# Kernel optimization log

Hardware: AMD Instinct MI355X
Metric: run time of the kernel (lower is better)

Reference implementation:

```python
import jax, jax.numpy as jnp
import numpy as np

CLIP_LENGTH = 256.0
NUM_CLASSES = 21
OVERLAP_THRESH = 0.5
GAMMA = 2.0
ALPHA = 0.25
EPS = float(np.finfo(np.float32).eps)

B, K, N_GT = 32, 32768, 32


def setup_inputs() -> dict:
    key = jax.random.key(0)
    ks = jax.random.split(key, 9)
    loc_data = jax.random.uniform(ks[0], (B, K, 2), jnp.float32) * 64.0 + 1.0  # frame-unit offsets
    conf_data = jax.random.normal(ks[1], (B, K, NUM_CLASSES), jnp.float32)
    prop_loc_data = jax.random.normal(ks[2], (B, K, 2), jnp.float32)
    prop_conf_data = jax.random.normal(ks[3], (B, K, NUM_CLASSES), jnp.float32)
    center_data = jax.random.normal(ks[4], (B, K, 1), jnp.float32)
    priors = jax.random.uniform(ks[5], (K, 1), jnp.float32)  # normalized centers in [0,1]
    t0 = jax.random.uniform(ks[6], (B, N_GT), jnp.float32) * 0.8
    dur = jax.random.uniform(ks[7], (B, N_GT), jnp.float32) * 0.18 + 0.02
    t1 = jnp.minimum(t0 + dur, 1.0)
    labels = jax.random.randint(ks[8], (B, N_GT), 1, NUM_CLASSES).astype(jnp.float32)
    targets = jnp.stack([t0, t1, labels], axis=-1)  # [B, N, 3]
    return {"loc_data": loc_data, "conf_data": conf_data, "prop_loc_data": prop_loc_data,
            "prop_conf_data": prop_conf_data, "center_data": center_data,
            "priors": priors, "targets": targets}


def _calc_iou(pred, target):
    pl, pr = pred[..., 0], pred[..., 1]
    tl, tr = target[..., 0], target[..., 1]
    inter = jnp.minimum(pl, tl) + jnp.minimum(pr, tr)
    union = (pl + pr) + (tl + tr) - inter
    return inter / jnp.maximum(union, EPS)


def _giou_loss(pred, target):
    pl, pr = pred[..., 0], pred[..., 1]
    tl, tr = target[..., 0], target[..., 1]
    inter = jnp.minimum(pl, tl) + jnp.minimum(pr, tr)
    union = (pl + pr) + (tl + tr) - inter
    ious = inter / jnp.maximum(union, EPS)
    ac = jnp.maximum(pl, tl) + jnp.maximum(pr, tr)
    gious = ious - (ac - union) / jnp.maximum(ac, EPS)
    return 1.0 - gious


_ALPHA_VEC = jnp.full((NUM_CLASSES,), 1.0 - ALPHA, jnp.float32).at[0].set(ALPHA)


def _focal_sum(logits, tgt):
    # FocalLoss_Ori with pre-softmax inside MultiSegmentLoss; reduction=sum
    probs = jax.nn.softmax(logits, axis=-1)
    pt = jnp.take_along_axis(probs, tgt[..., None], axis=-1)[..., 0] + 1e-10
    return (-_ALPHA_VEC[tgt] * (1.0 - pt) ** GAMMA * jnp.log(pt)).sum()


def _match_targets(loc_data_ng, priors, targets):
    # everything here mirrors the torch.no_grad() matching block
    truths = targets[..., :2]                       # [B,N,2]
    labels = targets[..., 2].astype(jnp.int32)      # [B,N]
    center = priors[:, 0]                           # [K]
    left = (center[None, :, None] - truths[:, None, :, 0]) * CLIP_LENGTH   # [B,K,N]
    right = (truths[:, None, :, 1] - center[None, :, None]) * CLIP_LENGTH  # [B,K,N]
    maxn = CLIP_LENGTH * 2.0
    area = jnp.where((left < 0) | (right < 0), maxn, left + right)
    best_area = area.min(-1)                        # [B,K]
    best_idx = area.argmin(-1)                      # [B,K]
    t0 = jnp.take_along_axis(truths[..., 0], best_idx, axis=1)
    t1 = jnp.take_along_axis(truths[..., 1], best_idx, axis=1)
    loc_t = jnp.stack([(center[None, :] - t0) * CLIP_LENGTH,
                       (t1 - center[None, :]) * CLIP_LENGTH], axis=-1)     # [B,K,2]
    conf_t = jnp.take_along_axis(labels, best_idx, axis=1)
    conf_t = jnp.where(best_area >= maxn, 0, conf_t)                       # [B,K]
    iou = _calc_iou(loc_data_ng, loc_t)
    prop_conf_t = jnp.where(iou < OVERLAP_THRESH, 0, conf_t)
    prop_w = loc_data_ng[..., 0] + loc_data_ng[..., 1]
    prop_loc_t = (loc_t - loc_data_ng) / (0.5 * prop_w[..., None])
    return loc_t, conf_t, prop_loc_t, prop_conf_t


def reference(loc_data, conf_data, prop_loc_data, prop_conf_data, center_data, priors, targets):
    loc_t, conf_t, prop_loc_t, prop_conf_t = _match_targets(
        jax.lax.stop_gradient(loc_data), priors, targets)

    pos = conf_t > 0
    posf = pos.astype(loc_data.dtype)
    N = jnp.maximum(posf.sum(), 1.0)
    prop_pos = prop_conf_t > 0
    ppf = prop_pos.astype(loc_data.dtype)
    PN = jnp.maximum(ppf.sum(), 1.0)

    # GIoU localization loss over positives
    loss_l = (_giou_loss(loc_data, loc_t) * posf).sum() / N

    # L1 proposal refinement loss over proposal positives
    loss_prop_l = (jnp.abs(prop_loc_data - prop_loc_t).sum(-1) * ppf).sum() / PN

    # centerness BCE-with-logits against refined IoU, over positives
    prop_pre_w = loc_data[..., 0:1] + loc_data[..., 1:2]
    cur_loc_p = 0.5 * prop_pre_w * prop_loc_data + loc_data
    ious_ct = jnp.maximum(_calc_iou(cur_loc_p, loc_t), 0.0)
    x = center_data[..., 0]
    bce = jnp.maximum(x, 0.0) - x * ious_ct + jnp.log1p(jnp.exp(-jnp.abs(x)))
    loss_ct = (bce * posf).sum() / N

    # focal classification losses over all anchors
    loss_c = _focal_sum(conf_data, conf_t) / N
    loss_prop_c = _focal_sum(prop_conf_data, prop_conf_t) / PN

    return (loss_l, loss_c, loss_prop_l, loss_prop_c, loss_ct)
```

## Files before the change

### kernel.cpp

```cpp
#include <hip/hip_runtime.h>
#include <math.h>

#define NCLS 21
#define NGT 32
#define CLIPLEN 256.0f
#define MAXN 512.0f
#define FEPS 1.1920928955078125e-07f

#define ROWF 21
#define WCH (64 * ROWF)


__device__ __forceinline__ float fastrcp(float x) { return __builtin_amdgcn_rcpf(x); }

__device__ __forceinline__ void glds16(const float* g, float* l) {
    __builtin_amdgcn_global_load_lds(
        (const __attribute__((address_space(1))) void*)g,
        (__attribute__((address_space(3))) void*)l, 16, 0, 0);
}
__device__ __forceinline__ void glds4(const float* g, float* l) {
    __builtin_amdgcn_global_load_lds(
        (const __attribute__((address_space(1))) void*)g,
        (__attribute__((address_space(3))) void*)l, 4, 0, 0);
}

__device__ __forceinline__ void stage_rows(const float* g, float* l, int lane) {
#pragma unroll
    for (int i = 0; i < 5; ++i)
        glds16(g + i * 256 + lane * 4, l + i * 256);
    glds4(g + 1280 + lane, l + 1280);
}

__device__ __forceinline__ void load_row(const float* __restrict__ row, float* r) {
#pragma unroll
    for (int i = 0; i < NCLS; ++i) r[i] = row[i];
}

__device__ __forceinline__ float focal_from(const float* r, float rt, int tgt) {
    float m0 = fmaxf(fmaxf(r[0],  r[1]),  r[2]);
    float m1 = fmaxf(fmaxf(r[3],  r[4]),  r[5]);
    float m2 = fmaxf(fmaxf(r[6],  r[7]),  r[8]);
    float m3 = fmaxf(fmaxf(r[9],  r[10]), r[11]);
    float m4 = fmaxf(fmaxf(r[12], r[13]), r[14]);
    float m5 = fmaxf(fmaxf(r[15], r[16]), r[17]);
    float m6 = fmaxf(fmaxf(r[18], r[19]), r[20]);
    float ma = fmaxf(fmaxf(m0, m1), m2);
    float mb = fmaxf(fmaxf(m3, m4), m5);
    float m  = fmaxf(fmaxf(ma, mb), m6);

    float e[NCLS];
#pragma unroll
    for (int i = 0; i < NCLS; ++i) e[i] = __expf(r[i] - m);
    float s0 = (e[0] + e[1])  + (e[2] + e[3]);
    float s1 = (e[4] + e[5])  + (e[6] + e[7]);
    float s2 = (e[8] + e[9])  + (e[10] + e[11]);
    float s3 = (e[12] + e[13]) + (e[14] + e[15]);
    float s4 = (e[16] + e[17]) + (e[18] + e[19]);
    float s  = ((s0 + s1) + (s2 + s3)) + (s4 + e[20]);

    float pt  = __expf(rt - m) * fastrcp(s) + 1e-10f;
    float lpt = __logf(pt);
    float a   = (tgt == 0) ? 0.25f : 0.75f;
    float om  = 1.0f - pt;
    return -a * om * om * lpt;
}

template <bool PARTIALS>
__global__ __launch_bounds__(256, 7) void msl_main(
    const float* __restrict__ loc_data,
    const float* __restrict__ conf_data,
    const float* __restrict__ prop_loc_data,
    const float* __restrict__ prop_conf_data,
    const float* __restrict__ center_data,
    const float* __restrict__ priors,
    const float* __restrict__ targets,
    double* __restrict__ ws,
    int K, int nblk)
{
    __shared__ float s_cls[4][WCH];
    __shared__ float s_red[6 * 4];

    const int b    = blockIdx.y;
    const int tid  = threadIdx.x;
    const int lane = tid & 63;
    const int w    = tid >> 6;
    const int kblk = blockIdx.x * 256;
    const int k    = kblk + tid;
    const size_t idx = (size_t)b * K + k;

    const size_t chunk0 = ((size_t)b * K + kblk + w * 64) * ROWF;
    float* lbuf = &s_cls[w][0];

    const float  c   = priors[k];
    const float2 loc = ((const float2*)loc_data)[idx];
    const float2 plo = ((const float2*)prop_loc_data)[idx];
    const float  x   = center_data[idx];

    stage_rows(conf_data + chunk0, lbuf, lane);

    const float* tgs = targets + (size_t)b * (NGT * 3);
    float bestA = 3.0e38f;
    float bT0 = 0.0f, bT1 = 0.0f, bLb = 0.0f;
#pragma unroll
    for (int n = 0; n < NGT; ++n) {
        const float t0n = tgs[3 * n];
        const float t1n = tgs[3 * n + 1];
        const float lbn = tgs[3 * n + 2];
        const bool outside = (t0n > c) || (t1n < c);
        const float cand = outside ? MAXN : (t1n - t0n) * CLIPLEN;
        const bool better = cand < bestA;
        bestA = better ? cand : bestA;
        bT0   = better ? t0n  : bT0;
        bT1   = better ? t1n  : bT1;
        bLb   = better ? lbn  : bLb;
    }
    const float tl = (c - bT0) * CLIPLEN;
    const float tr = (bT1 - c) * CLIPLEN;
    int conf_t = (bestA >= MAXN) ? 0 : (int)bLb;

    const float pl = loc.x, pr = loc.y;

    const float inter = fminf(pl, tl) + fminf(pr, tr);
    const float uni   = pl + pr + tl + tr - inter;
    const float iou   = inter * fastrcp(fmaxf(uni, FEPS));

    const int prop_conf_t = (iou < 0.5f) ? 0 : conf_t;
    const float posf = (conf_t > 0) ? 1.0f : 0.0f;
    const float ppf  = (prop_conf_t > 0) ? 1.0f : 0.0f;

    const float ac   = fmaxf(pl, tl) + fmaxf(pr, tr);
    const float giou = iou - (ac - uni) * fastrcp(fmaxf(ac, FEPS));
    const float v_ll = (1.0f - giou) * posf;

    const float prop_w = pl + pr;
    const float inv_hw = 2.0f * fastrcp(prop_w);
    const float plt0 = (tl - pl) * inv_hw;
    const float plt1 = (tr - pr) * inv_hw;
    const float v_lpl = (fabsf(plo.x - plt0) + fabsf(plo.y - plt1)) * ppf;

    const float cur0 = 0.5f * prop_w * plo.x + pl;
    const float cur1 = 0.5f * prop_w * plo.y + pr;
    const float in2  = fminf(cur0, tl) + fminf(cur1, tr);
    const float un2  = cur0 + cur1 + tl + tr - in2;
    const float iou2 = fmaxf(in2 * fastrcp(fmaxf(un2, FEPS)), 0.0f);
    const float ebx  = __expf(-fabsf(x));
    const float bce  = fmaxf(x, 0.0f) - x * iou2 + __logf(1.0f + ebx);
    const float v_ct = bce * posf;

    asm volatile("s_waitcnt vmcnt(0)" ::: "memory");
    __builtin_amdgcn_sched_barrier(0);
    const float* rowp = lbuf + lane * ROWF;
    float rr[NCLS];
    load_row(rowp, rr);
    const float rt_c = rowp[conf_t];
    asm volatile("s_waitcnt lgkmcnt(0)" ::: "memory");
    __builtin_amdgcn_sched_barrier(0);

    stage_rows(prop_conf_data + chunk0, lbuf, lane);

    const float v_lc = focal_from(rr, rt_c, conf_t);

    asm volatile("s_waitcnt vmcnt(0)" ::: "memory");
    __builtin_amdgcn_sched_barrier(0);
    load_row(rowp, rr);
    const float rt_p = rowp[prop_conf_t];
    const float v_lpc = focal_from(rr, rt_p, prop_conf_t);

    float vals[6] = { v_ll, v_lc, v_lpl, v_lpc, v_ct, posf + 4096.0f * ppf };
#pragma unroll
    for (int i = 0; i < 6; ++i) {
        float v = vals[i];
#pragma unroll
        for (int off = 32; off > 0; off >>= 1) v += __shfl_xor(v, off);
        if (lane == 0) s_red[i * 4 + w] = v;
    }
    __syncthreads();
    if (tid == 0) {
        const int blk = blockIdx.y * gridDim.x + blockIdx.x;
#pragma unroll
        for (int i = 0; i < 5; ++i) {
            double s = (double)s_red[i * 4 + 0] + (double)s_red[i * 4 + 1]
                     + (double)s_red[i * 4 + 2] + (double)s_red[i * 4 + 3];
            if (PARTIALS) ws[(size_t)i * nblk + blk] = s;
            else          atomicAdd(&ws[i], s);
        }
        double ct = (double)s_red[5 * 4 + 0] + (double)s_red[5 * 4 + 1]
                  + (double)s_red[5 * 4 + 2] + (double)s_red[5 * 4 + 3];
        double pp = floor(ct / 4096.0);
        double ps = ct - 4096.0 * pp;
        if (PARTIALS) {
            ws[(size_t)5 * nblk + blk] = ps;
            ws[(size_t)6 * nblk + blk] = pp;
        } else {
            atomicAdd(&ws[5], ps);
            atomicAdd(&ws[6], pp);
        }
    }
}

__global__ __launch_bounds__(256) void msl_reduce(
    const double* __restrict__ p, int nblk, float* __restrict__ out)
{
    __shared__ double s_acc[7];
    __shared__ double s_w[4];
    const int tid  = threadIdx.x;
    const int lane = tid & 63;
    const int w    = tid >> 6;

    for (int i = 0; i < 7; ++i) {
        double v = 0.0;
        for (int j = tid; j < nblk; j += 256) v += p[(size_t)i * nblk + j];
#pragma unroll
        for (int off = 32; off > 0; off >>= 1) v += __shfl_xor(v, off);
        if (lane == 0) s_w[w] = v;
        __syncthreads();
        if (tid == 0) s_acc[i] = s_w[0] + s_w[1] + s_w[2] + s_w[3];
        __syncthreads();
    }
    if (tid == 0) {
        const double N  = fmax(s_acc[5], 1.0);
        const double PN = fmax(s_acc[6], 1.0);
        out[0] = (float)(s_acc[0] / N);
        out[1] = (float)(s_acc[1] / N);
        out[2] = (float)(s_acc[2] / PN);
        out[3] = (float)(s_acc[3] / PN);
        out[4] = (float)(s_acc[4] / N);
    }
}

__global__ void msl_finalize(const double* __restrict__ acc, float* __restrict__ out) {
    const double N  = fmax(acc[5], 1.0);
    const double PN = fmax(acc[6], 1.0);
    out[0] = (float)(acc[0] / N);
    out[1] = (float)(acc[1] / N);
    out[2] = (float)(acc[2] / PN);
    out[3] = (float)(acc[3] / PN);
    out[4] = (float)(acc[4] / N);
}

extern "C" void kernel_launch(void* const* d_in, const int* in_sizes, int n_in,
                              void* d_out, int out_size, void* d_ws, size_t ws_size,
                              hipStream_t stream) {
    const float* loc_data       = (const float*)d_in[0];
    const float* conf_data      = (const float*)d_in[1];
    const float* prop_loc_data  = (const float*)d_in[2];
    const float* prop_conf_data = (const float*)d_in[3];
    const float* center_data    = (const float*)d_in[4];
    const float* priors         = (const float*)d_in[5];
    const float* targets        = (const float*)d_in[6];
    float* out = (float*)d_out;

    const int K = in_sizes[5];
    const int B = in_sizes[6] / (NGT * 3);
    const int nblk = (K / 256) * B;

    double* ws = (double*)d_ws;
    dim3 grid(K / 256, B);

    if (ws_size >= (size_t)7 * nblk * sizeof(double)) {
        msl_main<true><<<grid, 256, 0, stream>>>(loc_data, conf_data, prop_loc_data,
                                                 prop_conf_data, center_data, priors,
                                                 targets, ws, K, nblk);
        msl_reduce<<<1, 256, 0, stream>>>(ws, nblk, out);
    } else {
        hipMemsetAsync(ws, 0, 7 * sizeof(double), stream);
        msl_main<false><<<grid, 256, 0, stream>>>(loc_data, conf_data, prop_loc_data,
                                                  prop_conf_data, center_data, priors,
                                                  targets, ws, K, nblk);
        msl_finalize<<<1, 1, 0, stream>>>(ws, out);
    }
}
```

Baseline: 68.38 us.

## Restructure main kernel into single-wave blocks with double-buffered chunk pipeline

The main kernel now uses 64-thread single-wave blocks. Each block walks 8 chunks of 64 anchors and double-buffers the conf and prop_conf rows in LDS through global_load_lds, so the loads for the next chunk are in flight while the current chunk is computed. Per-thread accumulators and a wave-only reduction replace the cross-wave LDS reduction and __syncthreads. The cost is lower occupancy (launch bounds 64,2, about 21 KB of LDS per block) and reliance on a hand-counted vmcnt(16) wait, which could under-wait if the compiler reorders or splits the loads.

```diff
diff --git a/kernel.cpp b/kernel.cpp
--- a/kernel.cpp
+++ b/kernel.cpp
@@ -31,9 +31,19 @@
     glds4(g + 1280 + lane, l + 1280);
 }
 
-__device__ __forceinline__ void load_row(const float* __restrict__ row, float* r) {
-#pragma unroll
-    for (int i = 0; i < NCLS; ++i) r[i] = row[i];
+__device__ __forceinline__ void issue_chunk(
+    const float* __restrict__ conf, const float* __restrict__ prop,
+    const float* __restrict__ loc,  const float* __restrict__ plo,
+    const float* __restrict__ ctr,  const float* __restrict__ pri,
+    size_t a, int k, int lane, float* bufc, float* bufp,
+    float& cc, float2& lc, float2& pc, float& xx)
+{
+    cc = pri[k + lane];
+    lc = ((const float2*)loc)[a + lane];
+    pc = ((const float2*)plo)[a + lane];
+    xx = ctr[a + lane];
+    stage_rows(conf + a * ROWF, bufc, lane);
+    stage_rows(prop + a * ROWF, bufp, lane);
 }
 
 __device__ __forceinline__ float focal_from(const float* r, float rt, int tgt) {
@@ -65,40 +75,11 @@
     return -a * om * om * lpt;
 }
 
-template <bool PARTIALS>
-__global__ __launch_bounds__(256, 7) void msl_main(
-    const float* __restrict__ loc_data,
-    const float* __restrict__ conf_data,
-    const float* __restrict__ prop_loc_data,
-    const float* __restrict__ prop_conf_data,
-    const float* __restrict__ center_data,
-    const float* __restrict__ priors,
-    const float* __restrict__ targets,
-    double* __restrict__ ws,
-    int K, int nblk)
+__device__ __forceinline__ void compute_chunk(
+    const float* __restrict__ tgs, const float* bufc, const float* bufp, int lane,
+    float c, float2 loc, float2 plo, float x,
+    float& aLL, float& aLC, float& aLPL, float& aLPC, float& aCT, float& aCN)
 {
-    __shared__ float s_cls[4][WCH];
-    __shared__ float s_red[6 * 4];
-
-    const int b    = blockIdx.y;
-    const int tid  = threadIdx.x;
-    const int lane = tid & 63;
-    const int w    = tid >> 6;
-    const int kblk = blockIdx.x * 256;
-    const int k    = kblk + tid;
-    const size_t idx = (size_t)b * K + k;
-
-    const size_t chunk0 = ((size_t)b * K + kblk + w * 64) * ROWF;
-    float* lbuf = &s_cls[w][0];
-
-    const float  c   = priors[k];
-    const float2 loc = ((const float2*)loc_data)[idx];
-    const float2 plo = ((const float2*)prop_loc_data)[idx];
-    const float  x   = center_data[idx];
-
-    stage_rows(conf_data + chunk0, lbuf, lane);
-
-    const float* tgs = targets + (size_t)b * (NGT * 3);
     float bestA = 3.0e38f;
     float bT0 = 0.0f, bT1 = 0.0f, bLb = 0.0f;
 #pragma unroll
@@ -116,7 +97,7 @@
     }
     const float tl = (c - bT0) * CLIPLEN;
     const float tr = (bT1 - c) * CLIPLEN;
-    int conf_t = (bestA >= MAXN) ? 0 : (int)bLb;
+    const int conf_t = (bestA >= MAXN) ? 0 : (int)bLb;
 
     const float pl = loc.x, pr = loc.y;
 
@@ -147,51 +128,110 @@
     const float bce  = fmaxf(x, 0.0f) - x * iou2 + __logf(1.0f + ebx);
     const float v_ct = bce * posf;
 
-    asm volatile("s_waitcnt vmcnt(0)" ::: "memory");
-    __builtin_amdgcn_sched_barrier(0);
-    const float* rowp = lbuf + lane * ROWF;
+    const float* rowc = bufc + lane * ROWF;
+    const float* rowp = bufp + lane * ROWF;
     float rr[NCLS];
-    load_row(rowp, rr);
-    const float rt_c = rowp[conf_t];
-    asm volatile("s_waitcnt lgkmcnt(0)" ::: "memory");
-    __builtin_amdgcn_sched_barrier(0);
-
-    stage_rows(prop_conf_data + chunk0, lbuf, lane);
-
+#pragma unroll
+    for (int i = 0; i < NCLS; ++i) rr[i] = rowc[i];
+    const float rt_c = rowc[conf_t];
     const float v_lc = focal_from(rr, rt_c, conf_t);
-
-    asm volatile("s_waitcnt vmcnt(0)" ::: "memory");
-    __builtin_amdgcn_sched_barrier(0);
-    load_row(rowp, rr);
+#pragma unroll
+    for (int i = 0; i < NCLS; ++i) rr[i] = rowp[i];
     const float rt_p = rowp[prop_conf_t];
     const float v_lpc = focal_from(rr, rt_p, prop_conf_t);
 
-    float vals[6] = { v_ll, v_lc, v_lpl, v_lpc, v_ct, posf + 4096.0f * ppf };
+    aLL  += v_ll;
+    aLC  += v_lc;
+    aLPL += v_lpl;
+    aLPC += v_lpc;
+    aCT  += v_ct;
+    aCN  += posf + 4096.0f * ppf;
+}
+
+template <int NC, bool PARTIALS>
+__global__ __launch_bounds__(64, 2) void msl_main(
+    const float* __restrict__ loc_data,
+    const float* __restrict__ conf_data,
+    const float* __restrict__ prop_loc_data,
+    const float* __restrict__ prop_conf_data,
+    const float* __restrict__ center_data,
+    const float* __restrict__ priors,
+    const float* __restrict__ targets,
+    double* __restrict__ ws,
+    int K, int nblk)
+{
+    __shared__ float sb[2][2][WCH];
+
+    const int b    = blockIdx.y;
+    const int bx   = blockIdx.x;
+    const int lane = threadIdx.x;
+    const int ci0  = bx * NC;
+    const float* tgs = targets + (size_t)b * (NGT * 3);
+    const size_t base = (size_t)b * K;
+
+    float cA, cB, xA, xB;
+    float2 locA, locB, ploA, ploB;
+    float aLL = 0, aLC = 0, aLPL = 0, aLPC = 0, aCT = 0, aCN = 0;
+
+    {
+        const int k0 = ci0 * 64;
+        issue_chunk(conf_data, prop_conf_data, loc_data, prop_loc_data,
+                    center_data, priors, base + k0, k0, lane,
+                    &sb[0][0][0], &sb[0][1][0], cA, locA, ploA, xA);
+    }
+
+    for (int t = 0; t < NC / 2; ++t) {
+        {
+            __builtin_amdgcn_sched_barrier(0);
+            const int k1 = (ci0 + 2 * t + 1) * 64;
+            issue_chunk(conf_data, prop_conf_data, loc_data, prop_loc_data,
+                        center_data, priors, base + k1, k1, lane,
+                        &sb[1][0][0], &sb[1][1][0], cB, locB, ploB, xB);
+            __builtin_amdgcn_sched_barrier(0);
+            asm volatile("s_waitcnt vmcnt(16)" ::: "memory");
+            __builtin_amdgcn_sched_barrier(0);
+        }
+        compute_chunk(tgs, &sb[0][0][0], &sb[0][1][0], lane,
+                      cA, locA, ploA, xA, aLL, aLC, aLPL, aLPC, aCT, aCN);
+
+        if (t < NC / 2 - 1) {
+            __builtin_amdgcn_sched_barrier(0);
+            const int k2 = (ci0 + 2 * t + 2) * 64;
+            issue_chunk(conf_data, prop_conf_data, loc_data, prop_loc_data,
+                        center_data, priors, base + k2, k2, lane,
+                        &sb[0][0][0], &sb[0][1][0], cA, locA, ploA, xA);
+            __builtin_amdgcn_sched_barrier(0);
+            asm volatile("s_waitcnt vmcnt(16)" ::: "memory");
+            __builtin_amdgcn_sched_barrier(0);
+        } else {
+            asm volatile("s_waitcnt vmcnt(0)" ::: "memory");
+            __builtin_amdgcn_sched_barrier(0);
+        }
+        compute_chunk(tgs, &sb[1][0][0], &sb[1][1][0], lane,
+                      cB, locB, ploB, xB, aLL, aLC, aLPL, aLPC, aCT, aCN);
+    }
+
+    float vals[6] = { aLL, aLC, aLPL, aLPC, aCT, aCN };
 #pragma unroll
     for (int i = 0; i < 6; ++i) {
         float v = vals[i];
 #pragma unroll
         for (int off = 32; off > 0; off >>= 1) v += __shfl_xor(v, off);
-        if (lane == 0) s_red[i * 4 + w] = v;
-    }
-    __syncthreads();
-    if (tid == 0) {
-        const int blk = blockIdx.y * gridDim.x + blockIdx.x;
-#pragma unroll
-        for (int i = 0; i < 5; ++i) {
-            double s = (double)s_red[i * 4 + 0] + (double)s_red[i * 4 + 1]
-                     + (double)s_red[i * 4 + 2] + (double)s_red[i * 4 + 3];
-            if (PARTIALS) ws[(size_t)i * nblk + blk] = s;
-            else          atomicAdd(&ws[i], s);
-        }
-        double ct = (double)s_red[5 * 4 + 0] + (double)s_red[5 * 4 + 1]
-                  + (double)s_red[5 * 4 + 2] + (double)s_red[5 * 4 + 3];
-        double pp = floor(ct / 4096.0);
-        double ps = ct - 4096.0 * pp;
+        vals[i] = v;
+    }
+    if (lane == 0) {
+        const int blk = b * gridDim.x + bx;
+        const double ct = (double)vals[5];
+        const double pp = floor(ct / 4096.0);
+        const double ps = ct - 4096.0 * pp;
         if (PARTIALS) {
+#pragma unroll
+            for (int i = 0; i < 5; ++i) ws[(size_t)i * nblk + blk] = (double)vals[i];
             ws[(size_t)5 * nblk + blk] = ps;
             ws[(size_t)6 * nblk + blk] = pp;
         } else {
+#pragma unroll
+            for (int i = 0; i < 5; ++i) atomicAdd(&ws[i], (double)vals[i]);
             atomicAdd(&ws[5], ps);
             atomicAdd(&ws[6], pp);
         }
@@ -252,21 +292,35 @@
 
     const int K = in_sizes[5];
     const int B = in_sizes[6] / (NGT * 3);
-    const int nblk = (K / 256) * B;
 
     double* ws = (double*)d_ws;
-    dim3 grid(K / 256, B);
+
+    const bool nc8 = (K % (64 * 8) == 0);
+    const int  NCv = nc8 ? 8 : 2;
+    const int  gx  = K / (64 * NCv);
+    const int  nblk = gx * B;
+    dim3 grid(gx, B);
 
     if (ws_size >= (size_t)7 * nblk * sizeof(double)) {
-        msl_main<true><<<grid, 256, 0, stream>>>(loc_data, conf_data, prop_loc_data,
-                                                 prop_conf_data, center_data, priors,
-                                                 targets, ws, K, nblk);
+        if (nc8)
+            msl_main<8, true><<<grid, 64, 0, stream>>>(loc_data, conf_data, prop_loc_data,
+                                                       prop_conf_data, center_data, priors,
+                                                       targets, ws, K, nblk);
+        else
+            msl_main<2, true><<<grid, 64, 0, stream>>>(loc_data, conf_data, prop_loc_data,
+                                                       prop_conf_data, center_data, priors,
+                                                       targets, ws, K, nblk);
         msl_reduce<<<1, 256, 0, stream>>>(ws, nblk, out);
     } else {
         hipMemsetAsync(ws, 0, 7 * sizeof(double), stream);
-        msl_main<false><<<grid, 256, 0, stream>>>(loc_data, conf_data, prop_loc_data,
-                                                  prop_conf_data, center_data, priors,
-                                                  targets, ws, K, nblk);
+        if (nc8)
+            msl_main<8, false><<<grid, 64, 0, stream>>>(loc_data, conf_data, prop_loc_data,
+                                                        prop_conf_data, center_data, priors,
+                                                        targets, ws, K, nblk);
+        else
+            msl_main<2, false><<<grid, 64, 0, stream>>>(loc_data, conf_data, prop_loc_data,
+                                                        prop_conf_data, center_data, priors,
+                                                        targets, ws, K, nblk);
         msl_finalize<<<1, 1, 0, stream>>>(ws, out);
     }
 }
```

After: 73.44 us. +7.4%, slower.

## Load class rows directly into registers instead of staging through LDS

Applied to the files above, without the earlier changes.

Replaces the global_load_lds staging of the conf and prop_conf rows with direct per-thread unaligned 16-byte vector loads into registers, issuing both rows up front. The target logit is now picked with a select chain instead of an LDS indexed read, and occupancy is lowered to 5 to make room for the extra registers. This removes the LDS round trips and waitcnt serialisation between the two rows. The cost is strided, non-coalesced global access (84-byte rows per lane) and more register pressure.

```diff
diff --git a/kernel.cpp b/kernel.cpp
--- a/kernel.cpp
+++ b/kernel.cpp
@@ -7,36 +7,28 @@
 #define MAXN 512.0f
 #define FEPS 1.1920928955078125e-07f
 
-#define ROWF 21
-#define WCH (64 * ROWF)
-
+
+typedef float f32x4 __attribute__((ext_vector_type(4)));
+typedef f32x4 f32x4_u __attribute__((aligned(4)));
 
 __device__ __forceinline__ float fastrcp(float x) { return __builtin_amdgcn_rcpf(x); }
 
-__device__ __forceinline__ void glds16(const float* g, float* l) {
-    __builtin_amdgcn_global_load_lds(
-        (const __attribute__((address_space(1))) void*)g,
-        (__attribute__((address_space(3))) void*)l, 16, 0, 0);
-}
-__device__ __forceinline__ void glds4(const float* g, float* l) {
-    __builtin_amdgcn_global_load_lds(
-        (const __attribute__((address_space(1))) void*)g,
-        (__attribute__((address_space(3))) void*)l, 4, 0, 0);
-}
-
-__device__ __forceinline__ void stage_rows(const float* g, float* l, int lane) {
-#pragma unroll
-    for (int i = 0; i < 5; ++i)
-        glds16(g + i * 256 + lane * 4, l + i * 256);
-    glds4(g + 1280 + lane, l + 1280);
-}
-
-__device__ __forceinline__ void load_row(const float* __restrict__ row, float* r) {
-#pragma unroll
-    for (int i = 0; i < NCLS; ++i) r[i] = row[i];
-}
-
-__device__ __forceinline__ float focal_from(const float* r, float rt, int tgt) {
+__device__ __forceinline__ void load_row21(const float* __restrict__ p, float* r) {
+    f32x4 v0 = *(const f32x4_u*)(p + 0);
+    f32x4 v1 = *(const f32x4_u*)(p + 4);
+    f32x4 v2 = *(const f32x4_u*)(p + 8);
+    f32x4 v3 = *(const f32x4_u*)(p + 12);
+    f32x4 v4 = *(const f32x4_u*)(p + 16);
+    float  v5 = p[20];
+    r[0]=v0.x; r[1]=v0.y; r[2]=v0.z; r[3]=v0.w;
+    r[4]=v1.x; r[5]=v1.y; r[6]=v1.z; r[7]=v1.w;
+    r[8]=v2.x; r[9]=v2.y; r[10]=v2.z; r[11]=v2.w;
+    r[12]=v3.x; r[13]=v3.y; r[14]=v3.z; r[15]=v3.w;
+    r[16]=v4.x; r[17]=v4.y; r[18]=v4.z; r[19]=v4.w;
+    r[20]=v5;
+}
+
+__device__ __forceinline__ float focal_reg(const float* r, int tgt) {
     float m0 = fmaxf(fmaxf(r[0],  r[1]),  r[2]);
     float m1 = fmaxf(fmaxf(r[3],  r[4]),  r[5]);
     float m2 = fmaxf(fmaxf(r[6],  r[7]),  r[8]);
@@ -58,6 +50,10 @@
     float s4 = (e[16] + e[17]) + (e[18] + e[19]);
     float s  = ((s0 + s1) + (s2 + s3)) + (s4 + e[20]);
 
+    float rt = 0.0f;
+#pragma unroll
+    for (int i = 0; i < NCLS; ++i) rt = (i == tgt) ? r[i] : rt;
+
     float pt  = __expf(rt - m) * fastrcp(s) + 1e-10f;
     float lpt = __logf(pt);
     float a   = (tgt == 0) ? 0.25f : 0.75f;
@@ -66,7 +62,7 @@
 }
 
 template <bool PARTIALS>
-__global__ __launch_bounds__(256, 7) void msl_main(
+__global__ __launch_bounds__(256, 5) void msl_main(
     const float* __restrict__ loc_data,
     const float* __restrict__ conf_data,
     const float* __restrict__ prop_loc_data,
@@ -77,26 +73,23 @@
     double* __restrict__ ws,
     int K, int nblk)
 {
-    __shared__ float s_cls[4][WCH];
     __shared__ float s_red[6 * 4];
 
     const int b    = blockIdx.y;
     const int tid  = threadIdx.x;
     const int lane = tid & 63;
     const int w    = tid >> 6;
-    const int kblk = blockIdx.x * 256;
-    const int k    = kblk + tid;
+    const int k    = blockIdx.x * 256 + tid;
     const size_t idx = (size_t)b * K + k;
-
-    const size_t chunk0 = ((size_t)b * K + kblk + w * 64) * ROWF;
-    float* lbuf = &s_cls[w][0];
 
     const float  c   = priors[k];
     const float2 loc = ((const float2*)loc_data)[idx];
     const float2 plo = ((const float2*)prop_loc_data)[idx];
     const float  x   = center_data[idx];
 
-    stage_rows(conf_data + chunk0, lbuf, lane);
+    float rc[NCLS], rp[NCLS];
+    load_row21(conf_data      + idx * NCLS, rc);
+    load_row21(prop_conf_data + idx * NCLS, rp);
 
     const float* tgs = targets + (size_t)b * (NGT * 3);
     float bestA = 3.0e38f;
@@ -116,7 +109,7 @@
     }
     const float tl = (c - bT0) * CLIPLEN;
     const float tr = (bT1 - c) * CLIPLEN;
-    int conf_t = (bestA >= MAXN) ? 0 : (int)bLb;
+    const int conf_t = (bestA >= MAXN) ? 0 : (int)bLb;
 
     const float pl = loc.x, pr = loc.y;
 
@@ -147,24 +140,8 @@
     const float bce  = fmaxf(x, 0.0f) - x * iou2 + __logf(1.0f + ebx);
     const float v_ct = bce * posf;
 
-    asm volatile("s_waitcnt vmcnt(0)" ::: "memory");
-    __builtin_amdgcn_sched_barrier(0);
-    const float* rowp = lbuf + lane * ROWF;
-    float rr[NCLS];
-    load_row(rowp, rr);
-    const float rt_c = rowp[conf_t];
-    asm volatile("s_waitcnt lgkmcnt(0)" ::: "memory");
-    __builtin_amdgcn_sched_barrier(0);
-
-    stage_rows(prop_conf_data + chunk0, lbuf, lane);
-
-    const float v_lc = focal_from(rr, rt_c, conf_t);
-
-    asm volatile("s_waitcnt vmcnt(0)" ::: "memory");
-    __builtin_amdgcn_sched_barrier(0);
-    load_row(rowp, rr);
-    const float rt_p = rowp[prop_conf_t];
-    const float v_lpc = focal_from(rr, rt_p, prop_conf_t);
+    const float v_lc  = focal_reg(rc, conf_t);
+    const float v_lpc = focal_reg(rp, prop_conf_t);
 
     float vals[6] = { v_ll, v_lc, v_lpl, v_lpc, v_ct, posf + 4096.0f * ppf };
 #pragma unroll
```

Measured after the change: 69.03 us. No clear change (+0.9%).
